# Kernel tuning notes

Hardware: AMD Instinct MI355X
Metric: run time of the kernel (lower is better)

## Reference

```python
import jax, jax.numpy as jnp
import numpy as np

B, C, H = 8, 768, 12
TH = TW = 16
SH = SW = 32
N = TH * TW + SH * SW  # 1280


def setup_inputs() -> dict:
    key = jax.random.key(0)
    k1, k2, k3 = jax.random.split(key, 3)
    return {
        "x": jax.random.normal(k1, (B, N, C), jnp.float32),
        "qkv_w": jax.random.normal(k2, (3 * C, C), jnp.float32) * 0.02,
        "proj_w": jax.random.normal(k3, (C, C), jnp.float32) * 0.02,
        "proj_b": jnp.zeros((C,), jnp.float32),
        "t_h": TH, "t_w": TW, "s_h": SH, "s_w": SW,
    }


def reference(x, qkv_w, proj_w, proj_b, t_h, t_w, s_h, s_w):
    Bb, Nn, Cc = x.shape
    hd = Cc // H
    scale = hd ** -0.5
    nt = t_h * t_w
    ns = s_h * s_w
    # qkv projection: torch Linear computes x @ W.T
    qkv = (x @ qkv_w.T).reshape(Bb, Nn, 3, H, hd).transpose(2, 0, 3, 1, 4)
    q, k, v = qkv[0], qkv[1], qkv[2]  # each [B, H, N, hd]
    q_mt, q_s = q[:, :, :nt], q[:, :, nt:]
    k_mt, v_mt = k[:, :, :nt], v[:, :, :nt]
    # template queries attend only to template keys
    attn_t = jax.nn.softmax(jnp.einsum('bhqd,bhkd->bhqk', q_mt, k_mt) * scale, axis=-1)
    x_mt = jnp.einsum('bhqk,bhkd->bhqd', attn_t, v_mt).transpose(0, 2, 1, 3).reshape(Bb, nt, Cc)
    # search queries attend to all (template + search) keys
    attn_s = jax.nn.softmax(jnp.einsum('bhqd,bhkd->bhqk', q_s, k) * scale, axis=-1)
    x_s = jnp.einsum('bhqk,bhkd->bhqd', attn_s, v).transpose(0, 2, 1, 3).reshape(Bb, ns, Cc)
    out = jnp.concatenate([x_mt, x_s], axis=1)
    out = out @ proj_w.T + proj_b
    return out
```

## Files before the change

kernel.cpp:

```cpp
#include <hip/hip_runtime.h>
#include <hip/hip_bf16.h>


typedef __attribute__((ext_vector_type(8))) short s8v;
typedef __attribute__((ext_vector_type(4))) float f4v;
typedef __attribute__((ext_vector_type(4))) unsigned short u4v;
typedef __attribute__((ext_vector_type(4))) unsigned int u4i;

#define MFMA16(a, b, c) __builtin_amdgcn_mfma_f32_16x16x32_bf16((a), (b), (c), 0, 0, 0)

#define QSCALE 0.1803368801f

__device__ __forceinline__ unsigned short f2bf(float f) {
  unsigned int u = __builtin_bit_cast(unsigned int, f);
  u += 0x7fffu + ((u >> 16) & 1u);
  return (unsigned short)(u >> 16);
}

__device__ __forceinline__ unsigned int pk2(float lo, float hi) {
  __hip_bfloat162 t = __float22bfloat162_rn(make_float2(lo, hi));
  unsigned int u;
  __builtin_memcpy(&u, &t, 4);
  return u;
}

__device__ __forceinline__ s8v pack8(const float* p0, const float* p1) {
  u4i pi;
  pi[0] = pk2(p0[0], p0[1]);
  pi[1] = pk2(p0[2], p0[3]);
  pi[2] = pk2(p1[0], p1[1]);
  pi[3] = pk2(p1[2], p1[3]);
  return __builtin_bit_cast(s8v, pi);
}

__global__ __launch_bounds__(256) void cvt3_kernel(const float* __restrict__ x,
                                                   const float* __restrict__ wq,
                                                   const float* __restrict__ wp,
                                                   unsigned short* __restrict__ xb,
                                                   unsigned short* __restrict__ wqb,
                                                   unsigned short* __restrict__ wpb) {
  int i = blockIdx.x * 256 + threadIdx.x;
  const float* src;
  unsigned short* dst;
  int j;
  if (i < 1966080) {
    src = x; dst = xb; j = i;
  } else if (i < 1966080 + 442368) {
    src = wq; dst = wqb; j = i - 1966080;
  } else {
    src = wp; dst = wpb; j = i - (1966080 + 442368);
  }
  f4v v = ((const f4v*)src)[j];
  u4v o;
  o[0] = f2bf(v[0]); o[1] = f2bf(v[1]); o[2] = f2bf(v[2]); o[3] = f2bf(v[3]);
  ((u4v*)dst)[j] = o;
}

__global__ __launch_bounds__(256) void gemm_qkv_kernel(
    const unsigned short* __restrict__ A,
    const unsigned short* __restrict__ Bm,
    unsigned short* __restrict__ qb, unsigned short* __restrict__ kb,
    unsigned short* __restrict__ vT) {
  const int K = 768;
  __shared__ __align__(16) unsigned short As[128 * 32];
  __shared__ __align__(16) unsigned short Bs[128 * 32];
  int tid = threadIdx.x;
  int wave = tid >> 6, lane = tid & 63;
  int quad = lane >> 4, l16 = lane & 15;
  int wm = wave >> 1, wn = wave & 1;
  int m0 = blockIdx.y * 128, n0 = blockIdx.x * 128;

  f4v acc[4][4];
#pragma unroll
  for (int i = 0; i < 4; ++i)
#pragma unroll
    for (int j = 0; j < 4; ++j) acc[i][j] = (f4v){0.f, 0.f, 0.f, 0.f};

  for (int kt = 0; kt < K; kt += 32) {
#pragma unroll
    for (int c = 0; c < 2; ++c) {
      int idx = c * 256 + tid;
      int row = idx >> 2;
      int col = (idx & 3) << 3;
      const unsigned short* ga = A + (size_t)(m0 + row) * K + (kt + col);
      const unsigned short* gb = Bm + (size_t)(n0 + row) * K + (kt + col);
      __builtin_amdgcn_global_load_lds(
          (const __attribute__((address_space(1))) unsigned int*)ga,
          (__attribute__((address_space(3))) unsigned int*)((char*)As + idx * 16), 16, 0, 0);
      __builtin_amdgcn_global_load_lds(
          (const __attribute__((address_space(1))) unsigned int*)gb,
          (__attribute__((address_space(3))) unsigned int*)((char*)Bs + idx * 16), 16, 0, 0);
    }
    __syncthreads();
    s8v af[4], bfr[4];
#pragma unroll
    for (int mi = 0; mi < 4; ++mi)
      af[mi] = *(const s8v*)&As[(wm * 64 + mi * 16 + l16) * 32 + quad * 8];
#pragma unroll
    for (int ni = 0; ni < 4; ++ni)
      bfr[ni] = *(const s8v*)&Bs[(wn * 64 + ni * 16 + l16) * 32 + quad * 8];
#pragma unroll
    for (int mi = 0; mi < 4; ++mi)
#pragma unroll
      for (int ni = 0; ni < 4; ++ni)
        acc[mi][ni] = MFMA16(af[mi], bfr[ni], acc[mi][ni]);
    __syncthreads();
  }

#pragma unroll
  for (int ni = 0; ni < 4; ++ni) {
    int gn = n0 + wn * 64 + ni * 16 + l16;
    int which = gn / 768;
    int oo = gn - which * 768;
    int hh = oo >> 6;
    int dd = oo & 63;
#pragma unroll
    for (int mi = 0; mi < 4; ++mi) {
#pragma unroll
      for (int r = 0; r < 4; ++r) {
        int gm = m0 + wm * 64 + mi * 16 + quad * 4 + r;
        int bb = gm / 1280;
        int nn = gm - bb * 1280;
        float v = acc[mi][ni][r];
        if (which == 0) {
          qb[(((size_t)bb * 12 + hh) * 1280 + nn) * 64 + dd] = f2bf(v * QSCALE);
        } else if (which == 1) {
          kb[(((size_t)bb * 12 + hh) * 1280 + nn) * 64 + dd] = f2bf(v);
        } else {
          vT[(((size_t)bb * 12 + hh) * 64 + dd) * 1280 + nn] = f2bf(v);
        }
      }
    }
  }
}

__global__ __launch_bounds__(256) void gemm_proj_kernel(
    const unsigned short* __restrict__ A,
    const unsigned short* __restrict__ Bm,
    const float* __restrict__ pb, float* __restrict__ out) {
  const int K = 768;
  __shared__ __align__(16) unsigned short As[128 * 32];
  __shared__ __align__(16) unsigned short Bs[128 * 32];
  int tid = threadIdx.x;
  int wave = tid >> 6, lane = tid & 63;
  int quad = lane >> 4, l16 = lane & 15;
  int wm = wave >> 1, wn = wave & 1;
  int m0 = blockIdx.y * 128, n0 = blockIdx.x * 128;

  f4v acc[4][4];
#pragma unroll
  for (int i = 0; i < 4; ++i)
#pragma unroll
    for (int j = 0; j < 4; ++j) acc[i][j] = (f4v){0.f, 0.f, 0.f, 0.f};

  for (int kt = 0; kt < K; kt += 32) {
#pragma unroll
    for (int c = 0; c < 2; ++c) {
      int idx = c * 256 + tid;
      int row = idx >> 2;
      int col = (idx & 3) << 3;
      const unsigned short* ga = A + (size_t)(m0 + row) * K + (kt + col);
      const unsigned short* gb = Bm + (size_t)(n0 + row) * K + (kt + col);
      __builtin_amdgcn_global_load_lds(
          (const __attribute__((address_space(1))) unsigned int*)ga,
          (__attribute__((address_space(3))) unsigned int*)((char*)As + idx * 16), 16, 0, 0);
      __builtin_amdgcn_global_load_lds(
          (const __attribute__((address_space(1))) unsigned int*)gb,
          (__attribute__((address_space(3))) unsigned int*)((char*)Bs + idx * 16), 16, 0, 0);
    }
    __syncthreads();
    s8v af[4], bfr[4];
#pragma unroll
    for (int mi = 0; mi < 4; ++mi)
      af[mi] = *(const s8v*)&As[(wm * 64 + mi * 16 + l16) * 32 + quad * 8];
#pragma unroll
    for (int ni = 0; ni < 4; ++ni)
      bfr[ni] = *(const s8v*)&Bs[(wn * 64 + ni * 16 + l16) * 32 + quad * 8];
#pragma unroll
    for (int mi = 0; mi < 4; ++mi)
#pragma unroll
      for (int ni = 0; ni < 4; ++ni)
        acc[mi][ni] = MFMA16(af[mi], bfr[ni], acc[mi][ni]);
    __syncthreads();
  }

#pragma unroll
  for (int ni = 0; ni < 4; ++ni) {
    int gn = n0 + wn * 64 + ni * 16 + l16;
    float bias = pb[gn];
#pragma unroll
    for (int mi = 0; mi < 4; ++mi)
#pragma unroll
      for (int r = 0; r < 4; ++r) {
        int gm = m0 + wm * 64 + mi * 16 + quad * 4 + r;
        out[(size_t)gm * 768 + gn] = acc[mi][ni][r] + bias;
      }
  }
}

__global__ __launch_bounds__(256) void attn_kernel(
    const unsigned short* __restrict__ qb, const unsigned short* __restrict__ kb,
    const unsigned short* __restrict__ vT, unsigned short* __restrict__ attnb) {
  const int NT = 1280, CC = 768;
  int bx = blockIdx.x;
  int h = blockIdx.y;
  int b = blockIdx.z;
  int nk, qstart;
  if (bx < 8) { nk = 1280; qstart = 256 + bx * 128; }
  else        { nk = 256;  qstart = (bx - 8) * 128; }
  int wave = threadIdx.x >> 6, lane = threadIdx.x & 63;
  int quad = lane >> 4, l16 = lane & 15;
  int qa = qstart + wave * 32;
  int ntiles = nk >> 6;

  const unsigned short* qp = qb + (((size_t)b * 12 + h) * NT + qa) * 64;
  const unsigned short* kp = kb + (((size_t)b * 12 + h) * NT) * 64;
  const unsigned short* vp = vT + (((size_t)b * 12 + h) * 64) * NT;

  __shared__ __align__(16) unsigned short Kl[2][8][512];
  __shared__ __align__(16) unsigned short Vl[2][8][512];

  s8v bq0 = *(const s8v*)(qp + l16 * 64 + quad * 8);
  s8v bq1 = *(const s8v*)(qp + l16 * 64 + 32 + quad * 8);
  s8v bq2 = *(const s8v*)(qp + (16 + l16) * 64 + quad * 8);
  s8v bq3 = *(const s8v*)(qp + (16 + l16) * 64 + 32 + quad * 8);

  int perm = ((l16 >> 2) << 3) + (l16 & 3);
  int f0 = wave * 2, f1 = wave * 2 + 1;
  int koffs0, koffs1, voffs0, voffs1;
  {
    int s = f0 >> 2, dh = (f0 >> 1) & 1, hh = f0 & 1;
    koffs0 = (s * 32 + hh * 4 + perm) * 64 + (dh * 4 + quad) * 8;
    s = f1 >> 2; dh = (f1 >> 1) & 1; hh = f1 & 1;
    koffs1 = (s * 32 + hh * 4 + perm) * 64 + (dh * 4 + quad) * 8;
    int dt = f0 >> 1, sv = f0 & 1;
    voffs0 = (dt * 16 + l16) * NT + sv * 32 + quad * 8;
    dt = f1 >> 1; sv = f1 & 1;
    voffs1 = (dt * 16 + l16) * NT + sv * 32 + quad * 8;
  }

#define STAGE(bfi, k0_)                                                                     \
  do {                                                                                      \
    __builtin_amdgcn_global_load_lds(                                                       \
        (const __attribute__((address_space(1))) unsigned int*)(kp + (size_t)(k0_)*64 +     \
                                                                koffs0),                    \
        (__attribute__((address_space(3))) unsigned int*)((char*)&Kl[bfi][f0][0] +          \
                                                          lane * 16),                       \
        16, 0, 0);                                                                          \
    __builtin_amdgcn_global_load_lds(                                                       \
        (const __attribute__((address_space(1))) unsigned int*)(kp + (size_t)(k0_)*64 +     \
                                                                koffs1),                    \
        (__attribute__((address_space(3))) unsigned int*)((char*)&Kl[bfi][f1][0] +          \
                                                          lane * 16),                       \
        16, 0, 0);                                                                          \
    __builtin_amdgcn_global_load_lds(                                                       \
        (const __attribute__((address_space(1))) unsigned int*)(vp + (size_t)(k0_) +        \
                                                                voffs0),                    \
        (__attribute__((address_space(3))) unsigned int*)((char*)&Vl[bfi][f0][0] +          \
                                                          lane * 16),                       \
        16, 0, 0);                                                                          \
    __builtin_amdgcn_global_load_lds(                                                       \
        (const __attribute__((address_space(1))) unsigned int*)(vp + (size_t)(k0_) +        \
                                                                voffs1),                    \
        (__attribute__((address_space(3))) unsigned int*)((char*)&Vl[bfi][f1][0] +          \
                                                          lane * 16),                       \
        16, 0, 0);                                                                          \
  } while (0)

  float la = 0.f, lb = 0.f;
  f4v Oa[4], Ob[4];
#pragma unroll
  for (int dt = 0; dt < 4; ++dt) {
    Oa[dt] = (f4v){0.f, 0.f, 0.f, 0.f};
    Ob[dt] = (f4v){0.f, 0.f, 0.f, 0.f};
  }

  STAGE(0, 0);

  for (int t = 0; t < ntiles; ++t) {
    __syncthreads();
    int bf = t & 1;
    if (t + 1 < ntiles) STAGE(bf ^ 1, (t + 1) * 64);

    s8v kf[8], vf[8];
#pragma unroll
    for (int f = 0; f < 8; ++f) kf[f] = *(const s8v*)&Kl[bf][f][lane * 8];
#pragma unroll
    for (int g = 0; g < 8; ++g) vf[g] = *(const s8v*)&Vl[bf][g][lane * 8];

#pragma unroll
    for (int s = 0; s < 2; ++s) {
      int s4 = s << 2;
      f4v s0a = {0.f, 0.f, 0.f, 0.f}, s1a = {0.f, 0.f, 0.f, 0.f};
      f4v s0b = {0.f, 0.f, 0.f, 0.f}, s1b = {0.f, 0.f, 0.f, 0.f};
      s0a = MFMA16(kf[s4 | 0], bq0, s0a);
      s0a = MFMA16(kf[s4 | 2], bq1, s0a);
      s1a = MFMA16(kf[s4 | 1], bq0, s1a);
      s1a = MFMA16(kf[s4 | 3], bq1, s1a);
      s0b = MFMA16(kf[s4 | 0], bq2, s0b);
      s0b = MFMA16(kf[s4 | 2], bq3, s0b);
      s1b = MFMA16(kf[s4 | 1], bq2, s1b);
      s1b = MFMA16(kf[s4 | 3], bq3, s1b);

      float p0a[4], p1a[4], p0b[4], p1b[4];
#pragma unroll
      for (int r = 0; r < 4; ++r) {
        p0a[r] = __builtin_amdgcn_exp2f(s0a[r]);
        p1a[r] = __builtin_amdgcn_exp2f(s1a[r]);
        p0b[r] = __builtin_amdgcn_exp2f(s0b[r]);
        p1b[r] = __builtin_amdgcn_exp2f(s1b[r]);
      }
      la += ((p0a[0] + p0a[1]) + (p0a[2] + p0a[3])) + ((p1a[0] + p1a[1]) + (p1a[2] + p1a[3]));
      lb += ((p0b[0] + p0b[1]) + (p0b[2] + p0b[3])) + ((p1b[0] + p1b[1]) + (p1b[2] + p1b[3]));

      s8v pa = pack8(p0a, p1a);
      s8v pbv = pack8(p0b, p1b);

#pragma unroll
      for (int dt = 0; dt < 4; ++dt) {
        Oa[dt] = MFMA16(vf[dt * 2 + s], pa, Oa[dt]);
        Ob[dt] = MFMA16(vf[dt * 2 + s], pbv, Ob[dt]);
      }
    }
  }
#undef STAGE

  la += __shfl_xor(la, 16, 64);
  la += __shfl_xor(la, 32, 64);
  lb += __shfl_xor(lb, 16, 64);
  lb += __shfl_xor(lb, 32, 64);
  float inva = 1.f / la, invb = 1.f / lb;

  size_t rowa = ((size_t)b * NT + qa + l16) * CC + h * 64;
  size_t rowb = ((size_t)b * NT + qa + 16 + l16) * CC + h * 64;
#pragma unroll
  for (int dt = 0; dt < 4; ++dt) {
    u4v ova, ovb;
#pragma unroll
    for (int r = 0; r < 4; ++r) {
      ova[r] = f2bf(Oa[dt][r] * inva);
      ovb[r] = f2bf(Ob[dt][r] * invb);
    }
    *(u4v*)(attnb + rowa + dt * 16 + quad * 4) = ova;
    *(u4v*)(attnb + rowb + dt * 16 + quad * 4) = ovb;
  }
}

extern "C" void kernel_launch(void* const* d_in, const int* in_sizes, int n_in,
                              void* d_out, int out_size, void* d_ws, size_t ws_size,
                              hipStream_t stream) {
  const float* x = (const float*)d_in[0];
  const float* qkv_w = (const float*)d_in[1];
  const float* proj_w = (const float*)d_in[2];
  const float* proj_b = (const float*)d_in[3];
  float* out = (float*)d_out;

  char* ws = (char*)d_ws;
  unsigned short* xb = (unsigned short*)(ws + 0);
  unsigned short* wqkvb = (unsigned short*)(ws + 15728640);
  unsigned short* wpb = (unsigned short*)(ws + 19267584);
  unsigned short* qb = (unsigned short*)(ws + 20447232);
  unsigned short* kbuf = (unsigned short*)(ws + 36175872);
  unsigned short* vT = (unsigned short*)(ws + 51904512);
  unsigned short* attnb = xb;

  cvt3_kernel<<<dim3(9984), 256, 0, stream>>>(x, qkv_w, proj_w, xb, wqkvb, wpb);

  gemm_qkv_kernel<<<dim3(18, 80), 256, 0, stream>>>(xb, wqkvb, qb, kbuf, vT);
  attn_kernel<<<dim3(10, 12, 8), 256, 0, stream>>>(qb, kbuf, vT, attnb);
  gemm_proj_kernel<<<dim3(6, 80), 256, 0, stream>>>(attnb, wpb, proj_b, out);
}
```

Baseline: 280.1 us.

## Double-buffer GEMM LDS tiles with fragment-ordered layout and single barrier

Both the QKV and projection GEMM kernels now double-buffer their LDS tiles, so the next K-slice is prefetched with global_load_lds while MFMAs run on the current one. The second barrier per iteration is dropped. The LDS layout is reorganised so each 16-row fragment is stored in the order the MFMA operand loads read it, which makes each lane's read a contiguous 16-byte chunk and should reduce bank conflicts. The cost is twice the LDS per block, which may lower occupancy, and the change relies on the single barrier being enough to keep the two buffers apart.

```diff
diff --git a/kernel.cpp b/kernel.cpp
--- a/kernel.cpp
+++ b/kernel.cpp
@@ -62,50 +62,65 @@
     unsigned short* __restrict__ qb, unsigned short* __restrict__ kb,
     unsigned short* __restrict__ vT) {
   const int K = 768;
-  __shared__ __align__(16) unsigned short As[128 * 32];
-  __shared__ __align__(16) unsigned short Bs[128 * 32];
+  const int NIT = 24;
+  __shared__ __align__(16) unsigned short As[2][8][512];
+  __shared__ __align__(16) unsigned short Bs[2][8][512];
   int tid = threadIdx.x;
   int wave = tid >> 6, lane = tid & 63;
   int quad = lane >> 4, l16 = lane & 15;
   int wm = wave >> 1, wn = wave & 1;
   int m0 = blockIdx.y * 128, n0 = blockIdx.x * 128;
 
+  int fr0 = wave * 2, fr1 = wave * 2 + 1;
+  size_t aoff0 = (size_t)(m0 + fr0 * 16 + l16) * K + quad * 8;
+  size_t aoff1 = (size_t)(m0 + fr1 * 16 + l16) * K + quad * 8;
+  size_t boff0 = (size_t)(n0 + fr0 * 16 + l16) * K + quad * 8;
+  size_t boff1 = (size_t)(n0 + fr1 * 16 + l16) * K + quad * 8;
+
+#define GSTAGE(bfi, kt_)                                                                    \
+  do {                                                                                      \
+    __builtin_amdgcn_global_load_lds(                                                       \
+        (const __attribute__((address_space(1))) unsigned int*)(A + aoff0 + (kt_)),         \
+        (__attribute__((address_space(3))) unsigned int*)((char*)&As[bfi][fr0][0] +         \
+                                                          lane * 16), 16, 0, 0);            \
+    __builtin_amdgcn_global_load_lds(                                                       \
+        (const __attribute__((address_space(1))) unsigned int*)(A + aoff1 + (kt_)),         \
+        (__attribute__((address_space(3))) unsigned int*)((char*)&As[bfi][fr1][0] +         \
+                                                          lane * 16), 16, 0, 0);            \
+    __builtin_amdgcn_global_load_lds(                                                       \
+        (const __attribute__((address_space(1))) unsigned int*)(Bm + boff0 + (kt_)),        \
+        (__attribute__((address_space(3))) unsigned int*)((char*)&Bs[bfi][fr0][0] +         \
+                                                          lane * 16), 16, 0, 0);            \
+    __builtin_amdgcn_global_load_lds(                                                       \
+        (const __attribute__((address_space(1))) unsigned int*)(Bm + boff1 + (kt_)),        \
+        (__attribute__((address_space(3))) unsigned int*)((char*)&Bs[bfi][fr1][0] +         \
+                                                          lane * 16), 16, 0, 0);            \
+  } while (0)
+
   f4v acc[4][4];
 #pragma unroll
   for (int i = 0; i < 4; ++i)
 #pragma unroll
     for (int j = 0; j < 4; ++j) acc[i][j] = (f4v){0.f, 0.f, 0.f, 0.f};
 
-  for (int kt = 0; kt < K; kt += 32) {
-#pragma unroll
-    for (int c = 0; c < 2; ++c) {
-      int idx = c * 256 + tid;
-      int row = idx >> 2;
-      int col = (idx & 3) << 3;
-      const unsigned short* ga = A + (size_t)(m0 + row) * K + (kt + col);
-      const unsigned short* gb = Bm + (size_t)(n0 + row) * K + (kt + col);
-      __builtin_amdgcn_global_load_lds(
-          (const __attribute__((address_space(1))) unsigned int*)ga,
-          (__attribute__((address_space(3))) unsigned int*)((char*)As + idx * 16), 16, 0, 0);
-      __builtin_amdgcn_global_load_lds(
-          (const __attribute__((address_space(1))) unsigned int*)gb,
-          (__attribute__((address_space(3))) unsigned int*)((char*)Bs + idx * 16), 16, 0, 0);
-    }
+  GSTAGE(0, 0);
+  for (int t = 0; t < NIT; ++t) {
     __syncthreads();
+    int bf = t & 1;
+    if (t + 1 < NIT) GSTAGE(bf ^ 1, (t + 1) * 32);
+
     s8v af[4], bfr[4];
 #pragma unroll
-    for (int mi = 0; mi < 4; ++mi)
-      af[mi] = *(const s8v*)&As[(wm * 64 + mi * 16 + l16) * 32 + quad * 8];
-#pragma unroll
-    for (int ni = 0; ni < 4; ++ni)
-      bfr[ni] = *(const s8v*)&Bs[(wn * 64 + ni * 16 + l16) * 32 + quad * 8];
+    for (int mi = 0; mi < 4; ++mi) af[mi] = *(const s8v*)&As[bf][wm * 4 + mi][lane * 8];
+#pragma unroll
+    for (int ni = 0; ni < 4; ++ni) bfr[ni] = *(const s8v*)&Bs[bf][wn * 4 + ni][lane * 8];
 #pragma unroll
     for (int mi = 0; mi < 4; ++mi)
 #pragma unroll
       for (int ni = 0; ni < 4; ++ni)
         acc[mi][ni] = MFMA16(af[mi], bfr[ni], acc[mi][ni]);
-    __syncthreads();
-  }
+  }
+#undef GSTAGE
 
 #pragma unroll
   for (int ni = 0; ni < 4; ++ni) {
@@ -139,50 +154,65 @@
     const unsigned short* __restrict__ Bm,
     const float* __restrict__ pb, float* __restrict__ out) {
   const int K = 768;
-  __shared__ __align__(16) unsigned short As[128 * 32];
-  __shared__ __align__(16) unsigned short Bs[128 * 32];
+  const int NIT = 24;
+  __shared__ __align__(16) unsigned short As[2][8][512];
+  __shared__ __align__(16) unsigned short Bs[2][8][512];
   int tid = threadIdx.x;
   int wave = tid >> 6, lane = tid & 63;
   int quad = lane >> 4, l16 = lane & 15;
   int wm = wave >> 1, wn = wave & 1;
   int m0 = blockIdx.y * 128, n0 = blockIdx.x * 128;
 
+  int fr0 = wave * 2, fr1 = wave * 2 + 1;
+  size_t aoff0 = (size_t)(m0 + fr0 * 16 + l16) * K + quad * 8;
+  size_t aoff1 = (size_t)(m0 + fr1 * 16 + l16) * K + quad * 8;
+  size_t boff0 = (size_t)(n0 + fr0 * 16 + l16) * K + quad * 8;
+  size_t boff1 = (size_t)(n0 + fr1 * 16 + l16) * K + quad * 8;
+
+#define GSTAGE(bfi, kt_)                                                                    \
+  do {                                                                                      \
+    __builtin_amdgcn_global_load_lds(                                                       \
+        (const __attribute__((address_space(1))) unsigned int*)(A + aoff0 + (kt_)),         \
+        (__attribute__((address_space(3))) unsigned int*)((char*)&As[bfi][fr0][0] +         \
+                                                          lane * 16), 16, 0, 0);            \
+    __builtin_amdgcn_global_load_lds(                                                       \
+        (const __attribute__((address_space(1))) unsigned int*)(A + aoff1 + (kt_)),         \
+        (__attribute__((address_space(3))) unsigned int*)((char*)&As[bfi][fr1][0] +         \
+                                                          lane * 16), 16, 0, 0);            \
+    __builtin_amdgcn_global_load_lds(                                                       \
+        (const __attribute__((address_space(1))) unsigned int*)(Bm + boff0 + (kt_)),        \
+        (__attribute__((address_space(3))) unsigned int*)((char*)&Bs[bfi][fr0][0] +         \
+                                                          lane * 16), 16, 0, 0);            \
+    __builtin_amdgcn_global_load_lds(                                                       \
+        (const __attribute__((address_space(1))) unsigned int*)(Bm + boff1 + (kt_)),        \
+        (__attribute__((address_space(3))) unsigned int*)((char*)&Bs[bfi][fr1][0] +         \
+                                                          lane * 16), 16, 0, 0);            \
+  } while (0)
+
   f4v acc[4][4];
 #pragma unroll
   for (int i = 0; i < 4; ++i)
 #pragma unroll
     for (int j = 0; j < 4; ++j) acc[i][j] = (f4v){0.f, 0.f, 0.f, 0.f};
 
-  for (int kt = 0; kt < K; kt += 32) {
-#pragma unroll
-    for (int c = 0; c < 2; ++c) {
-      int idx = c * 256 + tid;
-      int row = idx >> 2;
-      int col = (idx & 3) << 3;
-      const unsigned short* ga = A + (size_t)(m0 + row) * K + (kt + col);
-      const unsigned short* gb = Bm + (size_t)(n0 + row) * K + (kt + col);
-      __builtin_amdgcn_global_load_lds(
-          (const __attribute__((address_space(1))) unsigned int*)ga,
-          (__attribute__((address_space(3))) unsigned int*)((char*)As + idx * 16), 16, 0, 0);
-      __builtin_amdgcn_global_load_lds(
-          (const __attribute__((address_space(1))) unsigned int*)gb,
-          (__attribute__((address_space(3))) unsigned int*)((char*)Bs + idx * 16), 16, 0, 0);
-    }
+  GSTAGE(0, 0);
+  for (int t = 0; t < NIT; ++t) {
     __syncthreads();
+    int bf = t & 1;
+    if (t + 1 < NIT) GSTAGE(bf ^ 1, (t + 1) * 32);
+
     s8v af[4], bfr[4];
 #pragma unroll
-    for (int mi = 0; mi < 4; ++mi)
-      af[mi] = *(const s8v*)&As[(wm * 64 + mi * 16 + l16) * 32 + quad * 8];
-#pragma unroll
-    for (int ni = 0; ni < 4; ++ni)
-      bfr[ni] = *(const s8v*)&Bs[(wn * 64 + ni * 16 + l16) * 32 + quad * 8];
+    for (int mi = 0; mi < 4; ++mi) af[mi] = *(const s8v*)&As[bf][wm * 4 + mi][lane * 8];
+#pragma unroll
+    for (int ni = 0; ni < 4; ++ni) bfr[ni] = *(const s8v*)&Bs[bf][wn * 4 + ni][lane * 8];
 #pragma unroll
     for (int mi = 0; mi < 4; ++mi)
 #pragma unroll
       for (int ni = 0; ni < 4; ++ni)
         acc[mi][ni] = MFMA16(af[mi], bfr[ni], acc[mi][ni]);
-    __syncthreads();
-  }
+  }
+#undef GSTAGE
 
 #pragma unroll
   for (int ni = 0; ni < 4; ++ni) {
@@ -245,26 +275,22 @@
         (const __attribute__((address_space(1))) unsigned int*)(kp + (size_t)(k0_)*64 +     \
                                                                 koffs0),                    \
         (__attribute__((address_space(3))) unsigned int*)((char*)&Kl[bfi][f0][0] +          \
-                                                          lane * 16),                       \
-        16, 0, 0);                                                                          \
+                                                          lane * 16), 16, 0, 0);            \
     __builtin_amdgcn_global_load_lds(                                                       \
         (const __attribute__((address_space(1))) unsigned int*)(kp + (size_t)(k0_)*64 +     \
                                                                 koffs1),                    \
         (__attribute__((address_space(3))) unsigned int*)((char*)&Kl[bfi][f1][0] +          \
-                                                          lane * 16),                       \
-        16, 0, 0);                                                                          \
+                                                          lane * 16), 16, 0, 0);            \
     __builtin_amdgcn_global_load_lds(                                                       \
         (const __attribute__((address_space(1))) unsigned int*)(vp + (size_t)(k0_) +        \
                                                                 voffs0),                    \
         (__attribute__((address_space(3))) unsigned int*)((char*)&Vl[bfi][f0][0] +          \
-                                                          lane * 16),                       \
-        16, 0, 0);                                                                          \
+                                                          lane * 16), 16, 0, 0);            \
     __builtin_amdgcn_global_load_lds(                                                       \
         (const __attribute__((address_space(1))) unsigned int*)(vp + (size_t)(k0_) +        \
                                                                 voffs1),                    \
         (__attribute__((address_space(3))) unsigned int*)((char*)&Vl[bfi][f1][0] +          \
-                                                          lane * 16),                       \
-        16, 0, 0);                                                                          \
+                                                          lane * 16), 16, 0, 0);            \
   } while (0)
 
   float la = 0.f, lb = 0.f;
```

After: 309.2 us. 10.4% more time.
